# Kernel tuning notes

Measured on AMD Instinct MI355X. Metric: run time of the kernel, lower is better.

The kernel has to match this reference:

```python
import jax, jax.numpy as jnp
import numpy as np

N_NODES = 100000
E = 500000
H = 128  # hidden_channels


def setup_inputs() -> dict:
    key = jax.random.key(0)
    ks = jax.random.split(key, 9)
    return {
        "z_pnode": jax.random.normal(ks[0], (N_NODES, H), dtype=jnp.float32),
        "z_onode": jax.random.normal(ks[1], (N_NODES, H), dtype=jnp.float32),
        "ptnp_edge_label_index": jax.random.randint(ks[2], (2, E), 0, N_NODES, dtype=jnp.int64) if jax.config.jax_enable_x64 else jax.random.randint(ks[2], (2, E), 0, N_NODES, dtype=jnp.int32),
        "nptp_edge_label_index": jax.random.randint(ks[3], (2, E), 0, N_NODES, dtype=jnp.int32),
        "nptnp_edge_label_index": jax.random.randint(ks[4], (2, E), 0, N_NODES, dtype=jnp.int32),
        "w1": jax.random.normal(ks[5], (2 * H, H), dtype=jnp.float32) * (1.0 / np.sqrt(2 * H)),
        "b1": jnp.zeros((H,), dtype=jnp.float32),
        "w2": jax.random.normal(ks[6], (H, 1), dtype=jnp.float32) * (1.0 / np.sqrt(H)),
        "b2": jnp.zeros((1,), dtype=jnp.float32),
    }


def reference(z_pnode, z_onode, ptnp_edge_label_index, nptp_edge_label_index,
              nptnp_edge_label_index, w1, b1, w2, b2):
    # Gather endpoint embeddings per edge type and concat along feature dim.
    z_ptnp = jnp.concatenate(
        [z_pnode[ptnp_edge_label_index[0]], z_onode[ptnp_edge_label_index[1]]], axis=-1)
    z_nptp = jnp.concatenate(
        [z_onode[nptp_edge_label_index[0]], z_pnode[nptp_edge_label_index[1]]], axis=-1)
    z_nptnp = jnp.concatenate(
        [z_onode[nptnp_edge_label_index[0]], z_onode[nptnp_edge_label_index[1]]], axis=-1)
    z = jnp.concatenate([z_ptnp, z_nptp, z_nptnp], axis=0)  # [3E, 2H]
    h = jax.nn.relu(z @ w1 + b1)                             # [3E, H]
    out = h @ w2 + b2                                        # [3E, 1]
    return out.reshape(-1)
```

## Files before the change

### kernel.cpp

```cpp
#include <hip/hip_runtime.h>
#include <hip/hip_bf16.h>
#include <stdint.h>

#define H 128
#define NNODES 100000
#define NEDGE 500000
#define MT 64

#define BSW_BYTES 65536
#define TBL_ELEMS (NNODES * H)
#define WS_NEEDED ((size_t)BSW_BYTES + 4ULL * TBL_ELEMS * 2ULL)

typedef __bf16 bf16x8 __attribute__((ext_vector_type(8)));
typedef float f32x4 __attribute__((ext_vector_type(4)));

union frag_cast { uint4 u; bf16x8 b; ushort s[8]; };

#define EPI_STRIDE 260

__device__ __forceinline__ ushort f2bf(float f) {
    __hip_bfloat16 h = __float2bfloat16(f);
    return *(ushort*)&h;
}

__device__ __forceinline__ void bf2_to_f(uint32_t u, float& lo, float& hi) {
    union { uint32_t i; float f; } a, b;
    a.i = u << 16;
    b.i = u & 0xffff0000u;
    lo = a.f;
    hi = b.f;
}

__global__ __launch_bounds__(256) void prep_bsw(const float* __restrict__ w1,
                                                ushort* __restrict__ bsw) {
    int i = blockIdx.x * 256 + threadIdx.x;
    int j = i & 7;
    int n = (i >> 3) & 255;
    int kb = i >> 11;
    int k = kb * 8 + j;
    int r = (n < 128) ? k : (128 + k);
    int c = n & 127;
    bsw[i] = f2bf(w1[r * H + c]);
}

__global__ __launch_bounds__(512) void gemm_tables(
    const float* __restrict__ zp, const float* __restrict__ zo,
    const ushort* __restrict__ bsw, const float* __restrict__ b1,
    ushort* __restrict__ t_ps, ushort* __restrict__ t_pd,
    ushort* __restrict__ t_os, ushort* __restrict__ t_od) {
    __shared__ ushort lds[MT * EPI_STRIDE];

    const int t = threadIdx.x;
    const int wave = t >> 6;
    const int lane = t & 63;
    const int l15 = lane & 15;
    const int quad = lane >> 4;
    const int R0 = (wave >> 2) * 32;
    const int col0 = (wave & 3) * 64;

    const int node0 = blockIdx.x * MT;
    const int zsel = blockIdx.y;
    const float* __restrict__ z = zsel ? zo : zp;

    frag_cast bfr[4][4];
#pragma unroll
    for (int s = 0; s < 4; ++s)
#pragma unroll
        for (int nt = 0; nt < 4; ++nt) {
            const int kb = s * 4 + quad;
            const int n = col0 + nt * 16 + l15;
            bfr[s][nt].u = *(const uint4*)(bsw + (kb * 256 + n) * 8);
        }

    f32x4 acc[2][4];
#pragma unroll
    for (int mt = 0; mt < 2; ++mt)
#pragma unroll
        for (int nt = 0; nt < 4; ++nt)
            acc[mt][nt] = (f32x4){0.f, 0.f, 0.f, 0.f};

#pragma unroll
    for (int s = 0; s < 4; ++s) {
#pragma unroll
        for (int mt = 0; mt < 2; ++mt) {
            int row_node = node0 + R0 + mt * 16 + l15;
            if (row_node >= NNODES) row_node = NNODES - 1;
            const float* p = z + (size_t)row_node * H + s * 32 + quad * 8;
            const float4 v0 = *(const float4*)p;
            const float4 v1 = *(const float4*)(p + 4);
            frag_cast a;
            a.s[0] = f2bf(v0.x); a.s[1] = f2bf(v0.y);
            a.s[2] = f2bf(v0.z); a.s[3] = f2bf(v0.w);
            a.s[4] = f2bf(v1.x); a.s[5] = f2bf(v1.y);
            a.s[6] = f2bf(v1.z); a.s[7] = f2bf(v1.w);
#pragma unroll
            for (int nt = 0; nt < 4; ++nt)
                acc[mt][nt] = __builtin_amdgcn_mfma_f32_16x16x32_bf16(
                    a.b, bfr[s][nt].b, acc[mt][nt], 0, 0, 0);
        }
    }

    float bias[4] = {0.f, 0.f, 0.f, 0.f};
    if ((wave & 3) >= 2) {
#pragma unroll
        for (int nt = 0; nt < 4; ++nt)
            bias[nt] = b1[(col0 - 128) + nt * 16 + l15];
    }

#pragma unroll
    for (int mt = 0; mt < 2; ++mt)
#pragma unroll
        for (int nt = 0; nt < 4; ++nt)
#pragma unroll
            for (int r = 0; r < 4; ++r) {
                const int row = R0 + mt * 16 + quad * 4 + r;
                const int col = col0 + nt * 16 + l15;
                lds[row * EPI_STRIDE + col] = f2bf(acc[mt][nt][r] + bias[nt]);
            }
    __syncthreads();

    const int table = t >> 8;
    const int tt = t & 255;
    const int row = tt >> 2;
    const int cbase = (tt & 3) * 32;
    if (node0 + row < NNODES) {
        ushort* __restrict__ dst =
            zsel ? (table ? t_od : t_os) : (table ? t_pd : t_ps);
        const size_t obase = (size_t)(node0 + row) * H + cbase;
        const int lbase = row * EPI_STRIDE + table * 128 + cbase;
#pragma unroll
        for (int q = 0; q < 4; ++q)
            *(uint4*)(dst + obase + q * 8) = *(const uint4*)(lds + lbase + q * 8);
    }
}

__global__ __launch_bounds__(256) void edge_kernel(
    const __hip_bfloat16* __restrict__ t_ps, const __hip_bfloat16* __restrict__ t_pd,
    const __hip_bfloat16* __restrict__ t_os, const __hip_bfloat16* __restrict__ t_od,
    const int* __restrict__ ptnp, const int* __restrict__ nptp,
    const int* __restrict__ nptnp,
    const float* __restrict__ w2, const float* __restrict__ b2,
    float* __restrict__ out) {
    const int tid = blockIdx.x * 256 + threadIdx.x;
    const int g = tid >> 4;
    const int lane = tid & 15;

    const __hip_bfloat16 *src_tbl, *dst_tbl;
    int si, di;
    if (g < NEDGE) {
        si = ptnp[g]; di = ptnp[NEDGE + g];
        src_tbl = t_ps; dst_tbl = t_od;
    } else if (g < 2 * NEDGE) {
        const int e = g - NEDGE;
        si = nptp[e]; di = nptp[NEDGE + e];
        src_tbl = t_os; dst_tbl = t_pd;
    } else {
        const int e = g - 2 * NEDGE;
        si = nptnp[e]; di = nptnp[NEDGE + e];
        src_tbl = t_os; dst_tbl = t_od;
    }

    const uint4 s4 = *(const uint4*)(src_tbl + si * H + lane * 8);
    const uint4 d4 = *(const uint4*)(dst_tbl + di * H + lane * 8);
    const float4 w2a = *(const float4*)(w2 + lane * 8);
    const float4 w2b = *(const float4*)(w2 + lane * 8 + 4);

    float s0, s1, d0, d1;
    float sum = 0.f;
    bf2_to_f(s4.x, s0, s1); bf2_to_f(d4.x, d0, d1);
    sum = fmaf(fmaxf(s0 + d0, 0.f), w2a.x, sum);
    sum = fmaf(fmaxf(s1 + d1, 0.f), w2a.y, sum);
    bf2_to_f(s4.y, s0, s1); bf2_to_f(d4.y, d0, d1);
    sum = fmaf(fmaxf(s0 + d0, 0.f), w2a.z, sum);
    sum = fmaf(fmaxf(s1 + d1, 0.f), w2a.w, sum);
    bf2_to_f(s4.z, s0, s1); bf2_to_f(d4.z, d0, d1);
    sum = fmaf(fmaxf(s0 + d0, 0.f), w2b.x, sum);
    sum = fmaf(fmaxf(s1 + d1, 0.f), w2b.y, sum);
    bf2_to_f(s4.w, s0, s1); bf2_to_f(d4.w, d0, d1);
    sum = fmaf(fmaxf(s0 + d0, 0.f), w2b.z, sum);
    sum = fmaf(fmaxf(s1 + d1, 0.f), w2b.w, sum);

    sum += __shfl_down(sum, 8, 16);
    sum += __shfl_down(sum, 4, 16);
    sum += __shfl_down(sum, 2, 16);
    sum += __shfl_down(sum, 1, 16);
    if (lane == 0) out[g] = sum + b2[0];
}

__global__ __launch_bounds__(128) void edge_direct(
    const float* __restrict__ zp, const float* __restrict__ zo,
    const int* __restrict__ ptnp, const int* __restrict__ nptp,
    const int* __restrict__ nptnp,
    const float* __restrict__ w1, const float* __restrict__ b1,
    const float* __restrict__ w2, const float* __restrict__ b2,
    float* __restrict__ out) {
    const int g = blockIdx.x;
    const int j = threadIdx.x;

    const float *src, *dst;
    int si, di;
    if (g < NEDGE) {
        si = ptnp[g]; di = ptnp[NEDGE + g]; src = zp; dst = zo;
    } else if (g < 2 * NEDGE) {
        const int e = g - NEDGE;
        si = nptp[e]; di = nptp[NEDGE + e]; src = zo; dst = zp;
    } else {
        const int e = g - 2 * NEDGE;
        si = nptnp[e]; di = nptnp[NEDGE + e]; src = zo; dst = zo;
    }
    const float* zs = src + si * H;
    const float* zd = dst + di * H;

    float acc = b1[j];
    for (int k = 0; k < H; ++k) acc = fmaf(zs[k], w1[k * H + j], acc);
    for (int k = 0; k < H; ++k) acc = fmaf(zd[k], w1[(H + k) * H + j], acc);
    float v = fmaxf(acc, 0.f) * w2[j];

    for (int off = 32; off > 0; off >>= 1) v += __shfl_down(v, off, 64);
    __shared__ float parts[2];
    if ((j & 63) == 0) parts[j >> 6] = v;
    __syncthreads();
    if (j == 0) out[g] = parts[0] + parts[1] + b2[0];
}

extern "C" void kernel_launch(void* const* d_in, const int* in_sizes, int n_in,
                              void* d_out, int out_size, void* d_ws, size_t ws_size,
                              hipStream_t stream) {
    const float* zp    = (const float*)d_in[0];
    const float* zo    = (const float*)d_in[1];
    const int*   ptnp  = (const int*)d_in[2];
    const int*   nptp  = (const int*)d_in[3];
    const int*   nptnp = (const int*)d_in[4];
    const float* w1    = (const float*)d_in[5];
    const float* b1    = (const float*)d_in[6];
    const float* w2    = (const float*)d_in[7];
    const float* b2    = (const float*)d_in[8];
    float* out = (float*)d_out;

    if (ws_size < WS_NEEDED) {
        edge_direct<<<3 * NEDGE, 128, 0, stream>>>(zp, zo, ptnp, nptp, nptnp,
                                                   w1, b1, w2, b2, out);
        return;
    }

    char* ws = (char*)d_ws;
    ushort* bsw = (ushort*)ws;
    ushort* t_ps = (ushort*)(ws + BSW_BYTES);
    ushort* t_pd = t_ps + TBL_ELEMS;
    ushort* t_os = t_pd + TBL_ELEMS;
    ushort* t_od = t_os + TBL_ELEMS;

    prep_bsw<<<128, 256, 0, stream>>>(w1, bsw);

    const int gx = (NNODES + MT - 1) / MT;
    gemm_tables<<<dim3(gx, 2), 512, 0, stream>>>(
        zp, zo, bsw, b1, t_ps, t_pd, t_os, t_od);

    const int total_threads = 3 * NEDGE * 16;
    edge_kernel<<<total_threads / 256, 256, 0, stream>>>(
        (const __hip_bfloat16*)t_ps, (const __hip_bfloat16*)t_pd,
        (const __hip_bfloat16*)t_os, (const __hip_bfloat16*)t_od,
        ptnp, nptp, nptnp, w2, b2, out);
}
```

Before: 312.4 us.

## Make node-table GEMM persistent with async global-to-LDS loads of input tiles

The node-table GEMM becomes a persistent kernel with a fixed grid of 256-thread blocks, each looping over 32-node tiles and keeping the W1 fragments in registers across tiles. Each fp32 input tile is staged into LDS with global_load_lds using an XOR swizzle, replacing per-lane direct global float4 loads. The LDS repack epilogue is dropped, and each lane now writes its bf16 outputs straight to global memory as scattered 2-byte stores. This is meant to cut B-fragment reloads and improve input-load efficiency, at the risk of poorly coalesced output writes and no overlap between tile loads and compute.

Result: faster. 270.5 us (-13.4%).

```diff
diff --git a/kernel.cpp b/kernel.cpp
--- a/kernel.cpp
+++ b/kernel.cpp
@@ -5,7 +5,9 @@
 #define H 128
 #define NNODES 100000
 #define NEDGE 500000
-#define MT 64
+#define MT 32
+#define TILES_PER_Z 3125
+#define GEMM_GRID 1024
 
 #define BSW_BYTES 65536
 #define TBL_ELEMS (NNODES * H)
@@ -15,8 +17,6 @@
 typedef float f32x4 __attribute__((ext_vector_type(4)));
 
 union frag_cast { uint4 u; bf16x8 b; ushort s[8]; };
-
-#define EPI_STRIDE 260
 
 __device__ __forceinline__ ushort f2bf(float f) {
     __hip_bfloat16 h = __float2bfloat16(f);
@@ -43,94 +43,102 @@
     bsw[i] = f2bf(w1[r * H + c]);
 }
 
-__global__ __launch_bounds__(512) void gemm_tables(
+__global__ __launch_bounds__(256, 3) void gemm_tables(
     const float* __restrict__ zp, const float* __restrict__ zo,
     const ushort* __restrict__ bsw, const float* __restrict__ b1,
     ushort* __restrict__ t_ps, ushort* __restrict__ t_pd,
     ushort* __restrict__ t_os, ushort* __restrict__ t_od) {
-    __shared__ ushort lds[MT * EPI_STRIDE];
+    __shared__ float abuf[MT * H];
 
     const int t = threadIdx.x;
     const int wave = t >> 6;
     const int lane = t & 63;
     const int l15 = lane & 15;
     const int quad = lane >> 4;
-    const int R0 = (wave >> 2) * 32;
-    const int col0 = (wave & 3) * 64;
-
-    const int node0 = blockIdx.x * MT;
-    const int zsel = blockIdx.y;
-    const float* __restrict__ z = zsel ? zo : zp;
+    const int n0 = wave * 64;
+    const int half = wave >> 1;
+    const int colbase = n0 - half * 128;
 
     frag_cast bfr[4][4];
 #pragma unroll
     for (int s = 0; s < 4; ++s)
 #pragma unroll
-        for (int nt = 0; nt < 4; ++nt) {
-            const int kb = s * 4 + quad;
-            const int n = col0 + nt * 16 + l15;
-            bfr[s][nt].u = *(const uint4*)(bsw + (kb * 256 + n) * 8);
+        for (int nt = 0; nt < 4; ++nt)
+            bfr[s][nt].u = *(const uint4*)(bsw + ((s * 4 + quad) * 256 + n0 + nt * 16 + l15) * 8);
+
+    float bias[4] = {0.f, 0.f, 0.f, 0.f};
+    if (half) {
+#pragma unroll
+        for (int nt = 0; nt < 4; ++nt)
+            bias[nt] = b1[colbase + nt * 16 + l15];
+    }
+
+    int src_off[4];
+    int lds_off[4];
+#pragma unroll
+    for (int i = 0; i < 4; ++i) {
+        const int r = (wave * 4 + i) * 2 + (lane >> 5);
+        const int jsrc = (lane & 31) ^ (r & 15);
+        src_off[i] = r * H + jsrc * 4;
+        lds_off[i] = (wave * 4 + i) * 256;
+    }
+
+    for (int tile = blockIdx.x; tile < 2 * TILES_PER_Z; tile += gridDim.x) {
+        const int zsel = tile & 1;
+        const int node0 = (tile >> 1) * MT;
+        const float* __restrict__ ztile =
+            (zsel ? zo : zp) + (size_t)node0 * H;
+
+#pragma unroll
+        for (int i = 0; i < 4; ++i) {
+            const float* gp = ztile + src_off[i];
+            float* lp = abuf + lds_off[i];
+            __builtin_amdgcn_global_load_lds(
+                (const __attribute__((address_space(1))) uint32_t*)gp,
+                (__attribute__((address_space(3))) uint32_t*)lp, 16, 0, 0);
         }
-
-    f32x4 acc[2][4];
-#pragma unroll
-    for (int mt = 0; mt < 2; ++mt)
-#pragma unroll
-        for (int nt = 0; nt < 4; ++nt)
-            acc[mt][nt] = (f32x4){0.f, 0.f, 0.f, 0.f};
-
-#pragma unroll
-    for (int s = 0; s < 4; ++s) {
-#pragma unroll
-        for (int mt = 0; mt < 2; ++mt) {
-            int row_node = node0 + R0 + mt * 16 + l15;
-            if (row_node >= NNODES) row_node = NNODES - 1;
-            const float* p = z + (size_t)row_node * H + s * 32 + quad * 8;
-            const float4 v0 = *(const float4*)p;
-            const float4 v1 = *(const float4*)(p + 4);
-            frag_cast a;
-            a.s[0] = f2bf(v0.x); a.s[1] = f2bf(v0.y);
-            a.s[2] = f2bf(v0.z); a.s[3] = f2bf(v0.w);
-            a.s[4] = f2bf(v1.x); a.s[5] = f2bf(v1.y);
-            a.s[6] = f2bf(v1.z); a.s[7] = f2bf(v1.w);
+        __syncthreads();
+
+        f32x4 acc[2][4];
+#pragma unroll
+        for (int mt = 0; mt < 2; ++mt)
 #pragma unroll
             for (int nt = 0; nt < 4; ++nt)
-                acc[mt][nt] = __builtin_amdgcn_mfma_f32_16x16x32_bf16(
-                    a.b, bfr[s][nt].b, acc[mt][nt], 0, 0, 0);
-        }
-    }
-
-    float bias[4] = {0.f, 0.f, 0.f, 0.f};
-    if ((wave & 3) >= 2) {
-#pragma unroll
-        for (int nt = 0; nt < 4; ++nt)
-            bias[nt] = b1[(col0 - 128) + nt * 16 + l15];
-    }
-
-#pragma unroll
-    for (int mt = 0; mt < 2; ++mt)
-#pragma unroll
-        for (int nt = 0; nt < 4; ++nt)
-#pragma unroll
-            for (int r = 0; r < 4; ++r) {
-                const int row = R0 + mt * 16 + quad * 4 + r;
-                const int col = col0 + nt * 16 + l15;
-                lds[row * EPI_STRIDE + col] = f2bf(acc[mt][nt][r] + bias[nt]);
+                acc[mt][nt] = (f32x4){0.f, 0.f, 0.f, 0.f};
+
+#pragma unroll
+        for (int s = 0; s < 4; ++s)
+#pragma unroll
+            for (int mt = 0; mt < 2; ++mt) {
+                const int row = mt * 16 + l15;
+                const int c = s * 4 + quad;
+                const float4 vlo = *(const float4*)(abuf + row * H + ((2 * c) ^ l15) * 4);
+                const float4 vhi = *(const float4*)(abuf + row * H + ((2 * c + 1) ^ l15) * 4);
+                frag_cast a;
+                a.s[0] = f2bf(vlo.x); a.s[1] = f2bf(vlo.y);
+                a.s[2] = f2bf(vlo.z); a.s[3] = f2bf(vlo.w);
+                a.s[4] = f2bf(vhi.x); a.s[5] = f2bf(vhi.y);
+                a.s[6] = f2bf(vhi.z); a.s[7] = f2bf(vhi.w);
+#pragma unroll
+                for (int nt = 0; nt < 4; ++nt)
+                    acc[mt][nt] = __builtin_amdgcn_mfma_f32_16x16x32_bf16(
+                        a.b, bfr[s][nt].b, acc[mt][nt], 0, 0, 0);
             }
-    __syncthreads();
-
-    const int table = t >> 8;
-    const int tt = t & 255;
-    const int row = tt >> 2;
-    const int cbase = (tt & 3) * 32;
-    if (node0 + row < NNODES) {
+        __syncthreads();
+
         ushort* __restrict__ dst =
-            zsel ? (table ? t_od : t_os) : (table ? t_pd : t_ps);
-        const size_t obase = (size_t)(node0 + row) * H + cbase;
-        const int lbase = row * EPI_STRIDE + table * 128 + cbase;
-#pragma unroll
-        for (int q = 0; q < 4; ++q)
-            *(uint4*)(dst + obase + q * 8) = *(const uint4*)(lds + lbase + q * 8);
+            zsel ? (half ? t_od : t_os) : (half ? t_pd : t_ps);
+#pragma unroll
+        for (int mt = 0; mt < 2; ++mt)
+#pragma unroll
+            for (int nt = 0; nt < 4; ++nt) {
+                const int col = colbase + nt * 16 + l15;
+#pragma unroll
+                for (int r = 0; r < 4; ++r) {
+                    const int grow = node0 + mt * 16 + quad * 4 + r;
+                    dst[(size_t)grow * H + col] = f2bf(acc[mt][nt][r] + bias[nt]);
+                }
+            }
     }
 }
 
@@ -252,8 +260,7 @@
 
     prep_bsw<<<128, 256, 0, stream>>>(w1, bsw);
 
-    const int gx = (NNODES + MT - 1) / MT;
-    gemm_tables<<<dim3(gx, 2), 512, 0, stream>>>(
+    gemm_tables<<<GEMM_GRID, 256, 0, stream>>>(
         zp, zo, bsw, b1, t_ps, t_pd, t_os, t_od);
 
     const int total_threads = 3 * NEDGE * 16;
```

## Persistent per-wave GEMM tiles and 4-edge-per-group edge kernel

Applied to the files above, without the earlier changes.

The table GEMM becomes a persistent grid of 1024 blocks. Each wave owns a 16-row tile across all 256 output columns, re-reads B fragments from global/L1 per step, and writes bf16 outputs directly without the LDS staging and block barrier. The edge kernel now handles four edges per 16-lane group, with vectorized int4 index loads, eight independent row gathers in flight and a single float4 output store. The aim is to cut synchronization and LDS traffic in the GEMM and to raise memory-level parallelism in the gather. The cost is uncoalesced 2-byte scattered stores in the GEMM epilogue, plus higher register pressure from 16 accumulators.

Result: slower. 454.2 us (+45.4%).

```diff
diff --git a/kernel.cpp b/kernel.cpp
--- a/kernel.cpp
+++ b/kernel.cpp
@@ -5,7 +5,9 @@
 #define H 128
 #define NNODES 100000
 #define NEDGE 500000
-#define MT 64
+#define GEMM_GRID 1024
+#define TILE_ROWS 16
+#define NTILES (2 * (NNODES / TILE_ROWS))
 
 #define BSW_BYTES 65536
 #define TBL_ELEMS (NNODES * H)
@@ -15,8 +17,6 @@
 typedef float f32x4 __attribute__((ext_vector_type(4)));
 
 union frag_cast { uint4 u; bf16x8 b; ushort s[8]; };
-
-#define EPI_STRIDE 260
 
 __device__ __forceinline__ ushort f2bf(float f) {
     __hip_bfloat16 h = __float2bfloat16(f);
@@ -43,49 +43,37 @@
     bsw[i] = f2bf(w1[r * H + c]);
 }
 
-__global__ __launch_bounds__(512) void gemm_tables(
+__global__ __launch_bounds__(256, 3) void gemm_tables(
     const float* __restrict__ zp, const float* __restrict__ zo,
     const ushort* __restrict__ bsw, const float* __restrict__ b1,
     ushort* __restrict__ t_ps, ushort* __restrict__ t_pd,
     ushort* __restrict__ t_os, ushort* __restrict__ t_od) {
-    __shared__ ushort lds[MT * EPI_STRIDE];
-
     const int t = threadIdx.x;
     const int wave = t >> 6;
     const int lane = t & 63;
     const int l15 = lane & 15;
     const int quad = lane >> 4;
-    const int R0 = (wave >> 2) * 32;
-    const int col0 = (wave & 3) * 64;
-
-    const int node0 = blockIdx.x * MT;
-    const int zsel = blockIdx.y;
-    const float* __restrict__ z = zsel ? zo : zp;
-
-    frag_cast bfr[4][4];
-#pragma unroll
-    for (int s = 0; s < 4; ++s)
-#pragma unroll
-        for (int nt = 0; nt < 4; ++nt) {
-            const int kb = s * 4 + quad;
-            const int n = col0 + nt * 16 + l15;
-            bfr[s][nt].u = *(const uint4*)(bsw + (kb * 256 + n) * 8);
-        }
-
-    f32x4 acc[2][4];
-#pragma unroll
-    for (int mt = 0; mt < 2; ++mt)
-#pragma unroll
-        for (int nt = 0; nt < 4; ++nt)
-            acc[mt][nt] = (f32x4){0.f, 0.f, 0.f, 0.f};
-
-#pragma unroll
-    for (int s = 0; s < 4; ++s) {
-#pragma unroll
-        for (int mt = 0; mt < 2; ++mt) {
-            int row_node = node0 + R0 + mt * 16 + l15;
-            if (row_node >= NNODES) row_node = NNODES - 1;
-            const float* p = z + (size_t)row_node * H + s * 32 + quad * 8;
+
+    const int wid = blockIdx.x * 4 + wave;
+    const int nw = gridDim.x * 4;
+
+    float bias[8];
+#pragma unroll
+    for (int i = 0; i < 8; ++i) bias[i] = b1[i * 16 + l15];
+
+    for (int tile = wid; tile < NTILES; tile += nw) {
+        const int zsel = tile & 1;
+        const int node0 = (tile >> 1) * TILE_ROWS;
+        const float* __restrict__ zrow =
+            (zsel ? zo : zp) + (size_t)node0 * H;
+
+        f32x4 acc[16];
+#pragma unroll
+        for (int nt = 0; nt < 16; ++nt) acc[nt] = (f32x4){0.f, 0.f, 0.f, 0.f};
+
+#pragma unroll
+        for (int s = 0; s < 4; ++s) {
+            const float* p = zrow + (size_t)l15 * H + s * 32 + quad * 8;
             const float4 v0 = *(const float4*)p;
             const float4 v1 = *(const float4*)(p + 4);
             frag_cast a;
@@ -93,44 +81,31 @@
             a.s[2] = f2bf(v0.z); a.s[3] = f2bf(v0.w);
             a.s[4] = f2bf(v1.x); a.s[5] = f2bf(v1.y);
             a.s[6] = f2bf(v1.z); a.s[7] = f2bf(v1.w);
-#pragma unroll
-            for (int nt = 0; nt < 4; ++nt)
-                acc[mt][nt] = __builtin_amdgcn_mfma_f32_16x16x32_bf16(
-                    a.b, bfr[s][nt].b, acc[mt][nt], 0, 0, 0);
+
+            const ushort* brow = bsw + (size_t)(s * 4 + quad) * 256 * 8 + l15 * 8;
+#pragma unroll
+            for (int nt = 0; nt < 16; ++nt) {
+                frag_cast b;
+                b.u = *(const uint4*)(brow + nt * 16 * 8);
+                acc[nt] = __builtin_amdgcn_mfma_f32_16x16x32_bf16(
+                    a.b, b.b, acc[nt], 0, 0, 0);
+            }
         }
-    }
-
-    float bias[4] = {0.f, 0.f, 0.f, 0.f};
-    if ((wave & 3) >= 2) {
-#pragma unroll
-        for (int nt = 0; nt < 4; ++nt)
-            bias[nt] = b1[(col0 - 128) + nt * 16 + l15];
-    }
-
-#pragma unroll
-    for (int mt = 0; mt < 2; ++mt)
-#pragma unroll
-        for (int nt = 0; nt < 4; ++nt)
+
+        ushort* __restrict__ stab = zsel ? t_os : t_ps;
+        ushort* __restrict__ dtab = zsel ? t_od : t_pd;
+#pragma unroll
+        for (int nt = 0; nt < 16; ++nt) {
+            const int col = nt * 16 + l15;
+            ushort* __restrict__ dst = (nt < 8) ? stab : dtab;
+            const int c = col & 127;
+            const float bb = (nt < 8) ? 0.f : bias[nt - 8];
 #pragma unroll
             for (int r = 0; r < 4; ++r) {
-                const int row = R0 + mt * 16 + quad * 4 + r;
-                const int col = col0 + nt * 16 + l15;
-                lds[row * EPI_STRIDE + col] = f2bf(acc[mt][nt][r] + bias[nt]);
+                const int grow = node0 + quad * 4 + r;
+                dst[(size_t)grow * H + c] = f2bf(acc[nt][r] + bb);
             }
-    __syncthreads();
-
-    const int table = t >> 8;
-    const int tt = t & 255;
-    const int row = tt >> 2;
-    const int cbase = (tt & 3) * 32;
-    if (node0 + row < NNODES) {
-        ushort* __restrict__ dst =
-            zsel ? (table ? t_od : t_os) : (table ? t_pd : t_ps);
-        const size_t obase = (size_t)(node0 + row) * H + cbase;
-        const int lbase = row * EPI_STRIDE + table * 128 + cbase;
-#pragma unroll
-        for (int q = 0; q < 4; ++q)
-            *(uint4*)(dst + obase + q * 8) = *(const uint4*)(lds + lbase + q * 8);
+        }
     }
 }
 
@@ -142,49 +117,72 @@
     const float* __restrict__ w2, const float* __restrict__ b2,
     float* __restrict__ out) {
     const int tid = blockIdx.x * 256 + threadIdx.x;
-    const int g = tid >> 4;
+    const int gg = tid >> 4;
+    if (gg >= (3 * NEDGE) / 4) return;
     const int lane = tid & 15;
+    const int e0 = gg * 4;
 
     const __hip_bfloat16 *src_tbl, *dst_tbl;
-    int si, di;
-    if (g < NEDGE) {
-        si = ptnp[g]; di = ptnp[NEDGE + g];
+    const int* idx;
+    int ebase;
+    if (e0 < NEDGE) {
+        idx = ptnp; ebase = e0;
         src_tbl = t_ps; dst_tbl = t_od;
-    } else if (g < 2 * NEDGE) {
-        const int e = g - NEDGE;
-        si = nptp[e]; di = nptp[NEDGE + e];
+    } else if (e0 < 2 * NEDGE) {
+        idx = nptp; ebase = e0 - NEDGE;
         src_tbl = t_os; dst_tbl = t_pd;
     } else {
-        const int e = g - 2 * NEDGE;
-        si = nptnp[e]; di = nptnp[NEDGE + e];
+        idx = nptnp; ebase = e0 - 2 * NEDGE;
         src_tbl = t_os; dst_tbl = t_od;
     }
 
-    const uint4 s4 = *(const uint4*)(src_tbl + si * H + lane * 8);
-    const uint4 d4 = *(const uint4*)(dst_tbl + di * H + lane * 8);
+    const int4 si = *(const int4*)(idx + ebase);
+    const int4 di = *(const int4*)(idx + NEDGE + ebase);
+
+    const uint4 s0 = *(const uint4*)(src_tbl + (size_t)si.x * H + lane * 8);
+    const uint4 d0 = *(const uint4*)(dst_tbl + (size_t)di.x * H + lane * 8);
+    const uint4 s1 = *(const uint4*)(src_tbl + (size_t)si.y * H + lane * 8);
+    const uint4 d1 = *(const uint4*)(dst_tbl + (size_t)di.y * H + lane * 8);
+    const uint4 s2 = *(const uint4*)(src_tbl + (size_t)si.z * H + lane * 8);
+    const uint4 d2 = *(const uint4*)(dst_tbl + (size_t)di.z * H + lane * 8);
+    const uint4 s3 = *(const uint4*)(src_tbl + (size_t)si.w * H + lane * 8);
+    const uint4 d3 = *(const uint4*)(dst_tbl + (size_t)di.w * H + lane * 8);
+
     const float4 w2a = *(const float4*)(w2 + lane * 8);
     const float4 w2b = *(const float4*)(w2 + lane * 8 + 4);
-
-    float s0, s1, d0, d1;
-    float sum = 0.f;
-    bf2_to_f(s4.x, s0, s1); bf2_to_f(d4.x, d0, d1);
-    sum = fmaf(fmaxf(s0 + d0, 0.f), w2a.x, sum);
-    sum = fmaf(fmaxf(s1 + d1, 0.f), w2a.y, sum);
-    bf2_to_f(s4.y, s0, s1); bf2_to_f(d4.y, d0, d1);
-    sum = fmaf(fmaxf(s0 + d0, 0.f), w2a.z, sum);
-    sum = fmaf(fmaxf(s1 + d1, 0.f), w2a.w, sum);
-    bf2_to_f(s4.z, s0, s1); bf2_to_f(d4.z, d0, d1);
-    sum = fmaf(fmaxf(s0 + d0, 0.f), w2b.x, sum);
-    sum = fmaf(fmaxf(s1 + d1, 0.f), w2b.y, sum);
-    bf2_to_f(s4.w, s0, s1); bf2_to_f(d4.w, d0, d1);
-    sum = fmaf(fmaxf(s0 + d0, 0.f), w2b.z, sum);
-    sum = fmaf(fmaxf(s1 + d1, 0.f), w2b.w, sum);
-
-    sum += __shfl_down(sum, 8, 16);
-    sum += __shfl_down(sum, 4, 16);
-    sum += __shfl_down(sum, 2, 16);
-    sum += __shfl_down(sum, 1, 16);
-    if (lane == 0) out[g] = sum + b2[0];
+    const float wv[8] = {w2a.x, w2a.y, w2a.z, w2a.w, w2b.x, w2b.y, w2b.z, w2b.w};
+
+    float sum[4] = {0.f, 0.f, 0.f, 0.f};
+    const uint4* sv[4] = {&s0, &s1, &s2, &s3};
+    const uint4* dv[4] = {&d0, &d1, &d2, &d3};
+#pragma unroll
+    for (int e = 0; e < 4; ++e) {
+        const uint32_t* su = (const uint32_t*)sv[e];
+        const uint32_t* du = (const uint32_t*)dv[e];
+        float acc = 0.f;
+#pragma unroll
+        for (int q = 0; q < 4; ++q) {
+            float a0, a1, b0, b1v;
+            bf2_to_f(su[q], a0, a1);
+            bf2_to_f(du[q], b0, b1v);
+            acc = fmaf(fmaxf(a0 + b0, 0.f), wv[2 * q], acc);
+            acc = fmaf(fmaxf(a1 + b1v, 0.f), wv[2 * q + 1], acc);
+        }
+        sum[e] = acc;
+    }
+
+#pragma unroll
+    for (int e = 0; e < 4; ++e) {
+        sum[e] += __shfl_down(sum[e], 8, 16);
+        sum[e] += __shfl_down(sum[e], 4, 16);
+        sum[e] += __shfl_down(sum[e], 2, 16);
+        sum[e] += __shfl_down(sum[e], 1, 16);
+    }
+    if (lane == 0) {
+        const float bb = b2[0];
+        float4 o = {sum[0] + bb, sum[1] + bb, sum[2] + bb, sum[3] + bb};
+        *(float4*)(out + e0) = o;
+    }
 }
 
 __global__ __launch_bounds__(128) void edge_direct(
@@ -252,12 +250,12 @@
 
     prep_bsw<<<128, 256, 0, stream>>>(w1, bsw);
 
-    const int gx = (NNODES + MT - 1) / MT;
-    gemm_tables<<<dim3(gx, 2), 512, 0, stream>>>(
+    gemm_tables<<<GEMM_GRID, 256, 0, stream>>>(
         zp, zo, bsw, b1, t_ps, t_pd, t_os, t_od);
 
-    const int total_threads = 3 * NEDGE * 16;
-    edge_kernel<<<total_threads / 256, 256, 0, stream>>>(
+    const int ngroups = (3 * NEDGE) / 4;
+    const int nblocks = (ngroups * 16 + 255) / 256;
+    edge_kernel<<<nblocks, 256, 0, stream>>>(
         (const __hip_bfloat16*)t_ps, (const __hip_bfloat16*)t_pd,
         (const __hip_bfloat16*)t_os, (const __hip_bfloat16*)t_od,
         ptnp, nptp, nptnp, w2, b2, out);
```
